# Optimization experiments

Hardware: AMD Instinct MI355X
Metric: run time of the kernel (lower is better)

Reference implementation:

```python
import jax, jax.numpy as jnp
import numpy as np

D_MODEL = 1024
N_HEAD = 16
D_HEAD = D_MODEL // N_HEAD
D_FF = 4096
EPS = 1e-5


def _layernorm(x, gamma, beta):
    mu = jnp.mean(x, axis=-1, keepdims=True)
    var = jnp.mean(jnp.square(x - mu), axis=-1, keepdims=True)
    return (x - mu) * jax.lax.rsqrt(var + EPS) * gamma + beta


def setup_inputs() -> dict:
    key = jax.random.key(0)
    ks = jax.random.split(key, 16)
    s = 1.0 / np.sqrt(D_MODEL)
    sf = 1.0 / np.sqrt(D_FF)
    return {
        "src": jax.random.normal(ks[0], (8, 1024, D_MODEL), dtype=jnp.float32),
        "Wq": jax.random.uniform(ks[1], (D_MODEL, D_MODEL), jnp.float32, -s, s),
        "bq": jnp.zeros((D_MODEL,), jnp.float32),
        "Wk": jax.random.uniform(ks[2], (D_MODEL, D_MODEL), jnp.float32, -s, s),
        "bk": jnp.zeros((D_MODEL,), jnp.float32),
        "Wv": jax.random.uniform(ks[3], (D_MODEL, D_MODEL), jnp.float32, -s, s),
        "bv": jnp.zeros((D_MODEL,), jnp.float32),
        "Wo": jax.random.uniform(ks[4], (D_MODEL, D_MODEL), jnp.float32, -s, s),
        "bo": jnp.zeros((D_MODEL,), jnp.float32),
        "W1": jax.random.uniform(ks[5], (D_MODEL, D_FF), jnp.float32, -s, s),
        "b1": jnp.zeros((D_FF,), jnp.float32),
        "W2": jax.random.uniform(ks[6], (D_FF, D_MODEL), jnp.float32, -sf, sf),
        "b2": jnp.zeros((D_MODEL,), jnp.float32),
        "g1": jnp.ones((D_MODEL,), jnp.float32),
        "beta1": jnp.zeros((D_MODEL,), jnp.float32),
        "g2": jnp.ones((D_MODEL,), jnp.float32),
        "beta2": jnp.zeros((D_MODEL,), jnp.float32),
    }


def reference(src, Wq, bq, Wk, bk, Wv, bv, Wo, bo, W1, b1, W2, b2, g1, beta1, g2, beta2):
    B, S, _ = src.shape
    x = _layernorm(src, g1, beta1)
    # QKV projections -> [B, H, S, Dh]
    def split_heads(t):
        return t.reshape(B, S, N_HEAD, D_HEAD).transpose(0, 2, 1, 3)
    q = split_heads(x @ Wq + bq)
    k = split_heads(x @ Wk + bk)
    v = split_heads(x @ Wv + bv)
    # SymbolicAttention (canonical graph): softmax(q k^T / sqrt(d_head)) v
    scores = jnp.einsum('bhqd,bhkd->bhqk', q, k) / np.sqrt(D_HEAD).astype(np.float32)
    attn = jax.nn.softmax(scores, axis=-1)
    ctx = jnp.einsum('bhqk,bhkd->bhqd', attn, v)
    ctx = ctx.transpose(0, 2, 1, 3).reshape(B, S, D_MODEL)
    src = src + (ctx @ Wo + bo)  # dropout is identity in eval
    y = _layernorm(src, g2, beta2)
    ffn = jax.nn.relu(y @ W1 + b1) @ W2 + b2
    return src + ffn
```

## Files before the change

### kernel.cpp

```cpp
#include <hip/hip_runtime.h>
#include <stdint.h>

#define D_MODEL 1024
#define N_HEAD  16
#define D_HEAD  64
#define D_FF    4096
#define SEQ     1024
#define BATCH   8
#define M_TOK   (BATCH*SEQ)

typedef __attribute__((ext_vector_type(8))) short bf16x8;
typedef __attribute__((ext_vector_type(4))) float f32x4;

__device__ __forceinline__ float bf2f(unsigned short u) {
    union { unsigned int u; float f; } x; x.u = ((unsigned int)u) << 16; return x.f;
}
__device__ __forceinline__ unsigned short f2bf(float f) {
    union { float f; unsigned int u; } x; x.f = f;
    unsigned int r = x.u + 0x7fffu + ((x.u >> 16) & 1u);
    return (unsigned short)(r >> 16);
}

typedef const __attribute__((address_space(1))) unsigned int* gas_t;
typedef __attribute__((address_space(3))) unsigned int* las_t;
__device__ __forceinline__ void gl_lds16(const unsigned short* g, unsigned short* l) {
    __builtin_amdgcn_global_load_lds((gas_t)g, (las_t)l, 16, 0, 0);
}

__global__ __launch_bounds__(256) void transpose_cvt(
        const float* __restrict__ src, unsigned short* __restrict__ dst,
        int R, int C)
{
    __shared__ float t[32][33];
    const int tx = threadIdx.x & 31, ty = threadIdx.x >> 5;
    const int c0 = blockIdx.x * 32, r0 = blockIdx.y * 32;
    #pragma unroll
    for (int i = 0; i < 32; i += 8)
        t[ty + i][tx] = src[(size_t)(r0 + ty + i) * C + c0 + tx];
    __syncthreads();
    #pragma unroll
    for (int i = 0; i < 32; i += 8)
        dst[(size_t)(c0 + ty + i) * R + r0 + tx] = f2bf(t[tx][ty + i]);
}

__global__ __launch_bounds__(256) void ln_kernel(
        const float* __restrict__ x, const float* __restrict__ g,
        const float* __restrict__ be, unsigned short* __restrict__ out)
{
    const int row = blockIdx.x, tid = threadIdx.x;
    const f32x4 v = *(const f32x4*)(x + (size_t)row * D_MODEL + tid * 4);
    float s  = v[0] + v[1] + v[2] + v[3];
    float ss = v[0]*v[0] + v[1]*v[1] + v[2]*v[2] + v[3]*v[3];
    #pragma unroll
    for (int o = 1; o < 64; o <<= 1) { s += __shfl_xor(s, o); ss += __shfl_xor(ss, o); }
    __shared__ float sa[4], sb[4];
    const int wv = tid >> 6;
    if ((tid & 63) == 0) { sa[wv] = s; sb[wv] = ss; }
    __syncthreads();
    s  = sa[0] + sa[1] + sa[2] + sa[3];
    ss = sb[0] + sb[1] + sb[2] + sb[3];
    const float mu   = s * (1.0f / D_MODEL);
    const float rstd = rsqrtf(ss * (1.0f / D_MODEL) - mu * mu + 1e-5f);
    const f32x4 gv = *(const f32x4*)(g  + tid * 4);
    const f32x4 bv = *(const f32x4*)(be + tid * 4);
    unsigned short w[4];
    #pragma unroll
    for (int j = 0; j < 4; j++) w[j] = f2bf((v[j] - mu) * rstd * gv[j] + bv[j]);
    *(uint2*)(out + (size_t)row * D_MODEL + tid * 4) = *(uint2*)w;
}

template<int MODE>
__global__ __launch_bounds__(512, 2) void gemm256(
        const unsigned short* __restrict__ A,
        const unsigned short* __restrict__ BT,
        const float* __restrict__ b1_,
        const float* __restrict__ b2_,
        const float* __restrict__ b3_,
        void* __restrict__ Cout,
        int M, int N, int K)
{
    (void)M;
    __shared__ unsigned short As[32768];
    __shared__ unsigned short Bs[32768];

    const int tid  = threadIdx.x;
    const int wave = tid >> 6, lane = tid & 63;
    const int quad = lane >> 4, l16 = lane & 15;
    const int wm = wave >> 2, wn = wave & 3;

    const int m0 = blockIdx.y * 256;
    const int n0 = blockIdx.x * 256;
    const int NT = K >> 6;

    const int st_row = tid >> 3;
    const int st_g   = (tid & 7) ^ (st_row & 7);
    const unsigned short* gA = A  + (size_t)(m0 + st_row) * K + st_g * 8;
    const unsigned short* gB = BT + (size_t)(n0 + st_row) * K + st_g * 8;
    unsigned short* lA = As + wave * 512;
    unsigned short* lB = Bs + wave * 512;

    const int aOff = (wm * 64 + l16) * 64;
    const int bOff = (wn * 32 + l16) * 64;
    const int s0s  = (quad ^ (l16 & 7)) * 8;
    const int s1s  = s0s ^ 32;

    f32x4 acc[8][4] = {};

#define STAGE_A(T, H, D) \
    do { gl_lds16(gA + (size_t)((H)*128   )*K + (size_t)(T)*64, lA + (D)*16384 + (H)*8192); \
         gl_lds16(gA + (size_t)((H)*128+64)*K + (size_t)(T)*64, lA + (D)*16384 + (H)*8192 + 4096); } while(0)
#define STAGE_B(T, H, D) \
    do { gl_lds16(gB + (size_t)((H)*128   )*K + (size_t)(T)*64, lB + (D)*16384 + (H)*8192); \
         gl_lds16(gB + (size_t)((H)*128+64)*K + (size_t)(T)*64, lB + (D)*16384 + (H)*8192 + 4096); } while(0)

    STAGE_A(0, 0, 0); STAGE_B(0, 0, 0); STAGE_B(0, 1, 0); STAGE_A(0, 1, 0);
    STAGE_A(1, 0, 1); STAGE_B(1, 0, 1); STAGE_B(1, 1, 1);
    asm volatile("s_waitcnt vmcnt(6)" ::: "memory");
    __builtin_amdgcn_s_barrier();
    asm volatile("" ::: "memory");

    for (int t = 0; t < NT; ++t) {
        const int db = t & 1;
        const unsigned short* Adb = As + db * 16384;
        const unsigned short* Bdb = Bs + db * 16384;
        bf16x8 af[4][2], bfA[2][2], bfB[2][2];

        #pragma unroll
        for (int mi = 0; mi < 4; ++mi) {
            af[mi][0] = *(const bf16x8*)(Adb + aOff + mi * 1024 + s0s);
            af[mi][1] = *(const bf16x8*)(Adb + aOff + mi * 1024 + s1s);
        }
        #pragma unroll
        for (int ni = 0; ni < 2; ++ni) {
            bfA[ni][0] = *(const bf16x8*)(Bdb + bOff + ni * 1024 + s0s);
            bfA[ni][1] = *(const bf16x8*)(Bdb + bOff + ni * 1024 + s1s);
        }
        if (t + 1 < NT) STAGE_A(t + 1, 1, db ^ 1);
        asm volatile("" ::: "memory");
        __builtin_amdgcn_s_barrier();
        asm volatile("s_waitcnt lgkmcnt(0)");
        __builtin_amdgcn_s_setprio(1);
        #pragma unroll
        for (int mi = 0; mi < 4; ++mi)
            #pragma unroll
            for (int ni = 0; ni < 2; ++ni) {
                acc[mi][ni] = __builtin_amdgcn_mfma_f32_16x16x32_bf16(
                        bfA[ni][0], af[mi][0], acc[mi][ni], 0, 0, 0);
                acc[mi][ni] = __builtin_amdgcn_mfma_f32_16x16x32_bf16(
                        bfA[ni][1], af[mi][1], acc[mi][ni], 0, 0, 0);
            }
        __builtin_amdgcn_s_setprio(0);
        asm volatile("" ::: "memory");
        __builtin_amdgcn_s_barrier();
        asm volatile("" ::: "memory");

        #pragma unroll
        for (int ni = 0; ni < 2; ++ni) {
            bfB[ni][0] = *(const bf16x8*)(Bdb + 8192 + bOff + ni * 1024 + s0s);
            bfB[ni][1] = *(const bf16x8*)(Bdb + 8192 + bOff + ni * 1024 + s1s);
        }
        if (t + 2 < NT) STAGE_A(t + 2, 0, db);
        asm volatile("" ::: "memory");
        __builtin_amdgcn_s_barrier();
        asm volatile("s_waitcnt lgkmcnt(0)");
        __builtin_amdgcn_s_setprio(1);
        #pragma unroll
        for (int mi = 0; mi < 4; ++mi)
            #pragma unroll
            for (int ni = 0; ni < 2; ++ni) {
                acc[mi][2 + ni] = __builtin_amdgcn_mfma_f32_16x16x32_bf16(
                        bfB[ni][0], af[mi][0], acc[mi][2 + ni], 0, 0, 0);
                acc[mi][2 + ni] = __builtin_amdgcn_mfma_f32_16x16x32_bf16(
                        bfB[ni][1], af[mi][1], acc[mi][2 + ni], 0, 0, 0);
            }
        __builtin_amdgcn_s_setprio(0);
        asm volatile("" ::: "memory");
        __builtin_amdgcn_s_barrier();
        asm volatile("" ::: "memory");

        #pragma unroll
        for (int mi = 0; mi < 4; ++mi) {
            af[mi][0] = *(const bf16x8*)(Adb + 8192 + aOff + mi * 1024 + s0s);
            af[mi][1] = *(const bf16x8*)(Adb + 8192 + aOff + mi * 1024 + s1s);
        }
        if (t + 2 < NT) STAGE_B(t + 2, 0, db);
        asm volatile("" ::: "memory");
        __builtin_amdgcn_s_barrier();
        asm volatile("s_waitcnt lgkmcnt(0)");
        __builtin_amdgcn_s_setprio(1);
        #pragma unroll
        for (int mi = 0; mi < 4; ++mi)
            #pragma unroll
            for (int ni = 0; ni < 2; ++ni) {
                acc[4 + mi][ni] = __builtin_amdgcn_mfma_f32_16x16x32_bf16(
                        bfA[ni][0], af[mi][0], acc[4 + mi][ni], 0, 0, 0);
                acc[4 + mi][ni] = __builtin_amdgcn_mfma_f32_16x16x32_bf16(
                        bfA[ni][1], af[mi][1], acc[4 + mi][ni], 0, 0, 0);
            }
        __builtin_amdgcn_s_setprio(0);
        asm volatile("" ::: "memory");
        __builtin_amdgcn_s_barrier();
        asm volatile("" ::: "memory");

        if (t + 2 < NT) {
            STAGE_B(t + 2, 1, db);
            asm volatile("s_waitcnt vmcnt(6)" ::: "memory");
        } else {
            asm volatile("s_waitcnt vmcnt(0)" ::: "memory");
        }
        __builtin_amdgcn_s_barrier();
        __builtin_amdgcn_s_setprio(1);
        #pragma unroll
        for (int mi = 0; mi < 4; ++mi)
            #pragma unroll
            for (int ni = 0; ni < 2; ++ni) {
                acc[4 + mi][2 + ni] = __builtin_amdgcn_mfma_f32_16x16x32_bf16(
                        bfB[ni][0], af[mi][0], acc[4 + mi][2 + ni], 0, 0, 0);
                acc[4 + mi][2 + ni] = __builtin_amdgcn_mfma_f32_16x16x32_bf16(
                        bfB[ni][1], af[mi][1], acc[4 + mi][2 + ni], 0, 0, 0);
            }
        __builtin_amdgcn_s_setprio(0);
        asm volatile("" ::: "memory");
        __builtin_amdgcn_s_barrier();
        asm volatile("" ::: "memory");
    }
#undef STAGE_A
#undef STAGE_B

    if (MODE == 1) {
        unsigned short* dst = (unsigned short*)Cout;
        #pragma unroll
        for (int f = 0; f < 8; ++f) {
            const int row = m0 + (f >> 2) * 128 + wm * 64 + (f & 3) * 16 + l16;
            #pragma unroll
            for (int g = 0; g < 4; ++g) {
                const int col = n0 + (g >> 1) * 128 + wn * 32 + (g & 1) * 16 + quad * 4;
                const f32x4 bs4 = *(const f32x4*)(b1_ + col);
                unsigned short w[4];
                #pragma unroll
                for (int r = 0; r < 4; ++r)
                    w[r] = f2bf(fmaxf(acc[f][g][r] + bs4[r], 0.0f));
                *(uint2*)(dst + (size_t)row * N + col) = *(uint2*)w;
            }
        }
    } else {
        const int rt = n0 >> 10;
        if (rt < 2) {
            unsigned short* dst = (unsigned short*)Cout + (size_t)rt * M_TOK * 1024;
            const float sc = (rt == 0) ? 0.125f : 1.0f;
            const float* bs = (rt == 0) ? b1_ : b2_;
            const int nb = n0 & 1023;
            #pragma unroll
            for (int f = 0; f < 8; ++f) {
                const int row = m0 + (f >> 2) * 128 + wm * 64 + (f & 3) * 16 + l16;
                #pragma unroll
                for (int g = 0; g < 4; ++g) {
                    const int col = nb + (g >> 1) * 128 + wn * 32 + (g & 1) * 16 + quad * 4;
                    const f32x4 bs4 = *(const f32x4*)(bs + col);
                    unsigned short w[4];
                    #pragma unroll
                    for (int r = 0; r < 4; ++r)
                        w[r] = f2bf((acc[f][g][r] + bs4[r]) * sc);
                    *(uint2*)(dst + (size_t)row * 1024 + col) = *(uint2*)w;
                }
            }
        } else {
            unsigned short* vdst = (unsigned short*)Cout + (size_t)2 * M_TOK * 1024;
            const int nb = n0 - 2048;
            #pragma unroll
            for (int f = 0; f < 8; ++f) {
                const int row = m0 + (f >> 2) * 128 + wm * 64 + (f & 3) * 16 + l16;
                const int bb = row >> 10, s = row & 1023;
                #pragma unroll
                for (int g = 0; g < 4; ++g) {
                    const int cc = nb + (g >> 1) * 128 + wn * 32 + (g & 1) * 16 + quad * 4;
                    #pragma unroll
                    for (int r = 0; r < 4; ++r)
                        vdst[((size_t)(bb * 1024 + cc + r)) * 1024 + s]
                            = f2bf(acc[f][g][r] + b3_[cc + r]);
                }
            }
        }
    }
}

template<int MODE>
__global__ __launch_bounds__(256) void gemm_bf16_tn(
        const unsigned short* __restrict__ A,
        const unsigned short* __restrict__ BT,
        const float* __restrict__ bias,
        const float* __restrict__ bias2,
        const float* __restrict__ bias3,
        const float* __restrict__ resid,
        void* __restrict__ Cout,
        int M, int N, int K)
{
    (void)bias2; (void)bias3;
    __shared__ unsigned short As[128 * 64];
    __shared__ unsigned short Bs[128 * 64];

    const int tid  = threadIdx.x;
    const int wave = tid >> 6, lane = tid & 63;
    const int quad = lane >> 4, l16 = lane & 15;

    int m0, n0;
    if (MODE == 2) {
        const int G = gridDim.x;
        const int f = blockIdx.x + G * blockIdx.y;
        m0 = ((f & 7) + 8 * ((f >> 3) / G)) * 128;
        n0 = ((f >> 3) % G) * 128;
    } else {
        m0 = blockIdx.y * 128;
        n0 = blockIdx.x * 128;
    }
    const int wm = (wave >> 1) * 64, wn = (wave & 1) * 64;

    const int st_row = wave * 8 + ((tid >> 3) & 7);
    const int st_g   = (tid & 7) ^ ((tid >> 3) & 7);
    const unsigned short* gA = A  + (size_t)(m0 + st_row) * K + st_g * 8;
    const unsigned short* gB = BT + (size_t)(n0 + st_row) * K + st_g * 8;
    unsigned short* lA = As + wave * 512;
    unsigned short* lB = Bs + wave * 512;
    const int rx = l16 & 7;

    f32x4 acc[4][4] = {};

    for (int k0 = 0; k0 < K; k0 += 64) {
        __syncthreads();
        #pragma unroll
        for (int j = 0; j < 4; j++) {
            gl_lds16(gA + (size_t)j * 32 * K + k0, lA + j * 2048);
            gl_lds16(gB + (size_t)j * 32 * K + k0, lB + j * 2048);
        }
        __syncthreads();

        #pragma unroll
        for (int h = 0; h < 2; h++) {
            bf16x8 af[4], bfr[4];
            #pragma unroll
            for (int mi = 0; mi < 4; mi++)
                af[mi] = *(const bf16x8*)(As + (wm + mi * 16 + l16) * 64
                                          + ((h * 4 + quad) ^ rx) * 8);
            #pragma unroll
            for (int ni = 0; ni < 4; ni++)
                bfr[ni] = *(const bf16x8*)(Bs + (wn + ni * 16 + l16) * 64
                                           + ((h * 4 + quad) ^ rx) * 8);
            #pragma unroll
            for (int mi = 0; mi < 4; mi++)
                #pragma unroll
                for (int ni = 0; ni < 4; ni++)
                    acc[mi][ni] = __builtin_amdgcn_mfma_f32_16x16x32_bf16(
                              bfr[ni], af[mi], acc[mi][ni], 0, 0, 0);
        }
    }

    #pragma unroll
    for (int mi = 0; mi < 4; mi++) {
        const int row = m0 + wm + mi * 16 + l16;
        #pragma unroll
        for (int ni = 0; ni < 4; ni++) {
            const int col = n0 + wn + ni * 16 + quad * 4;
            const f32x4 bs4 = *(const f32x4*)(bias + col);
            const f32x4 rv = *(const f32x4*)(resid + (size_t)row * N + col);
            f32x4 o;
            #pragma unroll
            for (int r = 0; r < 4; r++)
                o[r] = acc[mi][ni][r] + bs4[r] + rv[r];
            *(f32x4*)((float*)Cout + (size_t)row * N + col) = o;
        }
    }
}

#define ASTR 72
__global__ __launch_bounds__(256) void attn_mfma(
        const unsigned short* __restrict__ Q,
        const unsigned short* __restrict__ K,
        const unsigned short* __restrict__ VT,
        unsigned short* __restrict__ CTX)
{
    __shared__ unsigned short Ks[64 * ASTR];
    __shared__ unsigned short Vs[64 * ASTR];
    __shared__ unsigned short Ps[128 * ASTR];

    const int tid  = threadIdx.x;
    const int wave = tid >> 6, lane = tid & 63;
    const int quad = lane >> 4, l16 = lane & 15;
    const int bh = blockIdx.y;
    const int q0 = blockIdx.x * 128;
    const size_t baseQ = (size_t)(bh >> 4) * SEQ * D_MODEL + (size_t)(bh & 15) * D_HEAD;
    const size_t baseV = (size_t)bh * D_HEAD * SEQ;
    const int strip = wave * 32;

    bf16x8 qf[2][2];
    #pragma unroll
    for (int mt = 0; mt < 2; mt++)
        #pragma unroll
        for (int h = 0; h < 2; h++)
            qf[mt][h] = *(const bf16x8*)(Q + baseQ
                        + (size_t)(q0 + strip + mt * 16 + l16) * D_MODEL
                        + h * 32 + quad * 8);

    f32x4 of[2][4] = {};
    float l_p[2][4] = {};

    for (int c = 0; c < SEQ / 64; c++) {
        const int k0 = c * 64;
        __syncthreads();
        #pragma unroll
        for (int u = tid; u < 512; u += 256) {
            const int r = u >> 3, g = (u & 7) * 8;
            *(uint4*)(Ks + r * ASTR + g) =
                *(const uint4*)(K + baseQ + (size_t)(k0 + r) * D_MODEL + g);
            *(uint4*)(Vs + r * ASTR + g) =
                *(const uint4*)(VT + baseV + (size_t)r * SEQ + k0 + g);
        }
        __syncthreads();

        bf16x8 kf[4][2];
        #pragma unroll
        for (int kt = 0; kt < 4; kt++)
            #pragma unroll
            for (int h = 0; h < 2; h++)
                kf[kt][h] = *(const bf16x8*)(Ks + (kt * 16 + l16) * ASTR + h * 32 + quad * 8);

        #pragma unroll
        for (int mt = 0; mt < 2; mt++) {
            f32x4 s[4] = {};
            #pragma unroll
            for (int h = 0; h < 2; h++)
                #pragma unroll
                for (int kt = 0; kt < 4; kt++)
                    s[kt] = __builtin_amdgcn_mfma_f32_16x16x32_bf16(
                            qf[mt][h], kf[kt][h], s[kt], 0, 0, 0);
            #pragma unroll
            for (int kt = 0; kt < 4; kt++)
                #pragma unroll
                for (int r = 0; r < 4; r++) {
                    const float p = __expf(s[kt][r]);
                    l_p[mt][r] += p;
                    Ps[(strip + mt * 16 + quad * 4 + r) * ASTR + kt * 16 + l16] = f2bf(p);
                }
        }

        bf16x8 pf[2][2];
        #pragma unroll
        for (int mt = 0; mt < 2; mt++)
            #pragma unroll
            for (int h = 0; h < 2; h++)
                pf[mt][h] = *(const bf16x8*)(Ps + (strip + mt * 16 + l16) * ASTR
                                             + h * 32 + quad * 8);
        #pragma unroll
        for (int nt = 0; nt < 4; nt++) {
            bf16x8 vf[2];
            #pragma unroll
            for (int h = 0; h < 2; h++)
                vf[h] = *(const bf16x8*)(Vs + (nt * 16 + l16) * ASTR + h * 32 + quad * 8);
            #pragma unroll
            for (int mt = 0; mt < 2; mt++)
                #pragma unroll
                for (int h = 0; h < 2; h++)
                    of[mt][nt] = __builtin_amdgcn_mfma_f32_16x16x32_bf16(
                            pf[mt][h], vf[h], of[mt][nt], 0, 0, 0);
        }
    }

    #pragma unroll
    for (int mt = 0; mt < 2; mt++) {
        float inv[4];
        #pragma unroll
        for (int r = 0; r < 4; r++) {
            float l = l_p[mt][r];
            #pragma unroll
            for (int o = 1; o < 16; o <<= 1) l += __shfl_xor(l, o);
            inv[r] = 1.0f / l;
        }
        #pragma unroll
        for (int nt = 0; nt < 4; nt++)
            #pragma unroll
            for (int r = 0; r < 4; r++)
                CTX[baseQ + (size_t)(q0 + strip + mt * 16 + quad * 4 + r) * D_MODEL
                    + nt * 16 + l16] = f2bf(of[mt][nt][r] * inv[r]);
    }
}

extern "C" void kernel_launch(void* const* d_in, const int* in_sizes, int n_in,
                              void* d_out, int out_size, void* d_ws, size_t ws_size,
                              hipStream_t stream)
{
    (void)in_sizes; (void)n_in; (void)out_size; (void)ws_size;
    const float* src = (const float*)d_in[0];
    const float* Wq  = (const float*)d_in[1];
    const float* bq  = (const float*)d_in[2];
    const float* Wk  = (const float*)d_in[3];
    const float* bk  = (const float*)d_in[4];
    const float* Wv  = (const float*)d_in[5];
    const float* bv  = (const float*)d_in[6];
    const float* Wo  = (const float*)d_in[7];
    const float* bo  = (const float*)d_in[8];
    const float* W1  = (const float*)d_in[9];
    const float* b1  = (const float*)d_in[10];
    const float* W2  = (const float*)d_in[11];
    const float* b2  = (const float*)d_in[12];
    const float* g1  = (const float*)d_in[13];
    const float* be1 = (const float*)d_in[14];
    const float* g2  = (const float*)d_in[15];
    const float* be2 = (const float*)d_in[16];
    float* out = (float*)d_out;

    unsigned short* wqkvT = (unsigned short*)d_ws;
    unsigned short* woT = wqkvT + (size_t)3 * 1024 * 1024;
    unsigned short* w1T = woT + 1024 * 1024;
    unsigned short* w2T = w1T + (size_t)4096 * 1024;
    unsigned short* xn  = w2T + (size_t)1024 * 4096;
    unsigned short* q   = xn  + (size_t)M_TOK * D_MODEL;
    unsigned short* k   = q   + (size_t)M_TOK * D_MODEL;
    unsigned short* vT  = k   + (size_t)M_TOK * D_MODEL;
    unsigned short* ctx = vT  + (size_t)M_TOK * D_MODEL;
    unsigned short* hid = ctx + (size_t)M_TOK * D_MODEL;

    const dim3 blk(256);
    const dim3 blk512(512);

    transpose_cvt<<<dim3(32, 32),  blk, 0, stream>>>(Wq, wqkvT,                 1024, 1024);
    transpose_cvt<<<dim3(32, 32),  blk, 0, stream>>>(Wk, wqkvT + 1024 * 1024,   1024, 1024);
    transpose_cvt<<<dim3(32, 32),  blk, 0, stream>>>(Wv, wqkvT + 2 * 1024 * 1024, 1024, 1024);
    transpose_cvt<<<dim3(32, 32),  blk, 0, stream>>>(Wo, woT, 1024, 1024);
    transpose_cvt<<<dim3(128, 32), blk, 0, stream>>>(W1, w1T, 1024, 4096);
    transpose_cvt<<<dim3(32, 128), blk, 0, stream>>>(W2, w2T, 4096, 1024);

    ln_kernel<<<M_TOK, blk, 0, stream>>>(src, g1, be1, xn);

    gemm256<3><<<dim3(12, 32), blk512, 0, stream>>>(
        xn, wqkvT, bq, bk, bv, q, M_TOK, 3072, D_MODEL);

    attn_mfma<<<dim3(SEQ / 128, BATCH * N_HEAD), blk, 0, stream>>>(q, k, vT, ctx);

    gemm_bf16_tn<2><<<dim3(8, 64), blk, 0, stream>>>(
        ctx, woT, bo, nullptr, nullptr, src, out, M_TOK, D_MODEL, D_MODEL);

    ln_kernel<<<M_TOK, blk, 0, stream>>>(out, g2, be2, xn);

    gemm256<1><<<dim3(16, 32), blk512, 0, stream>>>(
        xn, w1T, b1, nullptr, nullptr, hid, M_TOK, D_FF, D_MODEL);

    gemm_bf16_tn<2><<<dim3(8, 64), blk, 0, stream>>>(
        hid, w2T, b2, nullptr, nullptr, out, out, M_TOK, D_MODEL, D_FF);
}
```

Measured before the change: 504.1 us.

## Use inline-asm LDS reads, reorder MFMAs, and remap blocks across XCDs in gemm256

The block index is remapped so consecutive tiles land in chunks per XCD (assuming 8 XCDs), which should improve L2 locality for shared A/B panels. LDS fragment loads become inline ds_read_b128 with immediate offsets from one base register, cutting address arithmetic. Sched barriers pin the order, and the MFMA loop order is changed so the two k-halves run as separate passes instead of back-to-back on the same accumulator. The asm reads hide dependencies from the compiler and assume the block count is divisible by 8.

```diff
diff --git a/kernel.cpp b/kernel.cpp
--- a/kernel.cpp
+++ b/kernel.cpp
@@ -26,6 +26,9 @@
 __device__ __forceinline__ void gl_lds16(const unsigned short* g, unsigned short* l) {
     __builtin_amdgcn_global_load_lds((gas_t)g, (las_t)l, 16, 0, 0);
 }
+
+#define DSR(dst, addr, IMM) \
+    asm volatile("ds_read_b128 %0, %1 offset:" #IMM : "=v"(dst) : "v"(addr))
 
 __global__ __launch_bounds__(256) void transpose_cvt(
         const float* __restrict__ src, unsigned short* __restrict__ dst,
@@ -88,8 +91,12 @@
     const int quad = lane >> 4, l16 = lane & 15;
     const int wm = wave >> 2, wn = wave & 3;
 
-    const int m0 = blockIdx.y * 256;
-    const int n0 = blockIdx.x * 256;
+    const int nbx = gridDim.x;
+    const int bid = blockIdx.x + nbx * blockIdx.y;
+    const int chunk = (nbx * gridDim.y) >> 3;
+    const int lg = (bid & 7) * chunk + (bid >> 3);
+    const int m0 = (lg / nbx) * 256;
+    const int n0 = (lg % nbx) * 256;
     const int NT = K >> 6;
 
     const int st_row = tid >> 3;
@@ -99,10 +106,12 @@
     unsigned short* lA = As + wave * 512;
     unsigned short* lB = Bs + wave * 512;
 
-    const int aOff = (wm * 64 + l16) * 64;
-    const int bOff = (wn * 32 + l16) * 64;
-    const int s0s  = (quad ^ (l16 & 7)) * 8;
-    const int s1s  = s0s ^ 32;
+    const unsigned asBase = (unsigned)(size_t)(las_t)(void*)As;
+    const unsigned bsBase = (unsigned)(size_t)(las_t)(void*)Bs;
+    const unsigned aOff = (unsigned)((wm * 64 + l16) * 128);
+    const unsigned bOff = (unsigned)((wn * 32 + l16) * 128);
+    const unsigned s0b  = (unsigned)((quad ^ (l16 & 7)) * 16);
+    const unsigned s1b  = s0b ^ 64;
 
     f32x4 acc[8][4] = {};
 
@@ -121,86 +130,90 @@
 
     for (int t = 0; t < NT; ++t) {
         const int db = t & 1;
-        const unsigned short* Adb = As + db * 16384;
-        const unsigned short* Bdb = Bs + db * 16384;
-        bf16x8 af[4][2], bfA[2][2], bfB[2][2];
-
-        #pragma unroll
-        for (int mi = 0; mi < 4; ++mi) {
-            af[mi][0] = *(const bf16x8*)(Adb + aOff + mi * 1024 + s0s);
-            af[mi][1] = *(const bf16x8*)(Adb + aOff + mi * 1024 + s1s);
-        }
-        #pragma unroll
-        for (int ni = 0; ni < 2; ++ni) {
-            bfA[ni][0] = *(const bf16x8*)(Bdb + bOff + ni * 1024 + s0s);
-            bfA[ni][1] = *(const bf16x8*)(Bdb + bOff + ni * 1024 + s1s);
-        }
+        const unsigned dbo = (unsigned)(db * 32768);
+        const unsigned aR0 = asBase + dbo + aOff + s0b;
+        const unsigned aR1 = asBase + dbo + aOff + s1b;
+        const unsigned bR0 = bsBase + dbo + bOff + s0b;
+        const unsigned bR1 = bsBase + dbo + bOff + s1b;
+        bf16x8 a0[4], a1[4], bA0[2], bA1[2], bB0[2], bB1[2];
+
+        DSR(a0[0], aR0, 0);    DSR(a0[1], aR0, 2048);
+        DSR(a0[2], aR0, 4096); DSR(a0[3], aR0, 6144);
+        DSR(a1[0], aR1, 0);    DSR(a1[1], aR1, 2048);
+        DSR(a1[2], aR1, 4096); DSR(a1[3], aR1, 6144);
+        DSR(bA0[0], bR0, 0);   DSR(bA0[1], bR0, 2048);
+        DSR(bA1[0], bR1, 0);   DSR(bA1[1], bR1, 2048);
         if (t + 1 < NT) STAGE_A(t + 1, 1, db ^ 1);
         asm volatile("" ::: "memory");
         __builtin_amdgcn_s_barrier();
-        asm volatile("s_waitcnt lgkmcnt(0)");
+        asm volatile("s_waitcnt lgkmcnt(0)" ::: "memory");
+        __builtin_amdgcn_sched_barrier(0);
         __builtin_amdgcn_s_setprio(1);
         #pragma unroll
         for (int mi = 0; mi < 4; ++mi)
             #pragma unroll
-            for (int ni = 0; ni < 2; ++ni) {
+            for (int ni = 0; ni < 2; ++ni)
                 acc[mi][ni] = __builtin_amdgcn_mfma_f32_16x16x32_bf16(
-                        bfA[ni][0], af[mi][0], acc[mi][ni], 0, 0, 0);
+                        bA0[ni], a0[mi], acc[mi][ni], 0, 0, 0);
+        #pragma unroll
+        for (int mi = 0; mi < 4; ++mi)
+            #pragma unroll
+            for (int ni = 0; ni < 2; ++ni)
                 acc[mi][ni] = __builtin_amdgcn_mfma_f32_16x16x32_bf16(
-                        bfA[ni][1], af[mi][1], acc[mi][ni], 0, 0, 0);
-            }
+                        bA1[ni], a1[mi], acc[mi][ni], 0, 0, 0);
         __builtin_amdgcn_s_setprio(0);
         asm volatile("" ::: "memory");
         __builtin_amdgcn_s_barrier();
-        asm volatile("" ::: "memory");
-
-        #pragma unroll
-        for (int ni = 0; ni < 2; ++ni) {
-            bfB[ni][0] = *(const bf16x8*)(Bdb + 8192 + bOff + ni * 1024 + s0s);
-            bfB[ni][1] = *(const bf16x8*)(Bdb + 8192 + bOff + ni * 1024 + s1s);
-        }
+
+        DSR(bB0[0], bR0, 16384);   DSR(bB0[1], bR0, 18432);
+        DSR(bB1[0], bR1, 16384);   DSR(bB1[1], bR1, 18432);
         if (t + 2 < NT) STAGE_A(t + 2, 0, db);
         asm volatile("" ::: "memory");
         __builtin_amdgcn_s_barrier();
-        asm volatile("s_waitcnt lgkmcnt(0)");
+        asm volatile("s_waitcnt lgkmcnt(0)" ::: "memory");
+        __builtin_amdgcn_sched_barrier(0);
         __builtin_amdgcn_s_setprio(1);
         #pragma unroll
         for (int mi = 0; mi < 4; ++mi)
             #pragma unroll
-            for (int ni = 0; ni < 2; ++ni) {
+            for (int ni = 0; ni < 2; ++ni)
                 acc[mi][2 + ni] = __builtin_amdgcn_mfma_f32_16x16x32_bf16(
-                        bfB[ni][0], af[mi][0], acc[mi][2 + ni], 0, 0, 0);
+                        bB0[ni], a0[mi], acc[mi][2 + ni], 0, 0, 0);
+        #pragma unroll
+        for (int mi = 0; mi < 4; ++mi)
+            #pragma unroll
+            for (int ni = 0; ni < 2; ++ni)
                 acc[mi][2 + ni] = __builtin_amdgcn_mfma_f32_16x16x32_bf16(
-                        bfB[ni][1], af[mi][1], acc[mi][2 + ni], 0, 0, 0);
-            }
+                        bB1[ni], a1[mi], acc[mi][2 + ni], 0, 0, 0);
         __builtin_amdgcn_s_setprio(0);
         asm volatile("" ::: "memory");
         __builtin_amdgcn_s_barrier();
-        asm volatile("" ::: "memory");
-
-        #pragma unroll
-        for (int mi = 0; mi < 4; ++mi) {
-            af[mi][0] = *(const bf16x8*)(Adb + 8192 + aOff + mi * 1024 + s0s);
-            af[mi][1] = *(const bf16x8*)(Adb + 8192 + aOff + mi * 1024 + s1s);
-        }
+
+        DSR(a0[0], aR0, 16384); DSR(a0[1], aR0, 18432);
+        DSR(a0[2], aR0, 20480); DSR(a0[3], aR0, 22528);
+        DSR(a1[0], aR1, 16384); DSR(a1[1], aR1, 18432);
+        DSR(a1[2], aR1, 20480); DSR(a1[3], aR1, 22528);
         if (t + 2 < NT) STAGE_B(t + 2, 0, db);
         asm volatile("" ::: "memory");
         __builtin_amdgcn_s_barrier();
-        asm volatile("s_waitcnt lgkmcnt(0)");
+        asm volatile("s_waitcnt lgkmcnt(0)" ::: "memory");
+        __builtin_amdgcn_sched_barrier(0);
         __builtin_amdgcn_s_setprio(1);
         #pragma unroll
         for (int mi = 0; mi < 4; ++mi)
             #pragma unroll
-            for (int ni = 0; ni < 2; ++ni) {
+            for (int ni = 0; ni < 2; ++ni)
                 acc[4 + mi][ni] = __builtin_amdgcn_mfma_f32_16x16x32_bf16(
-                        bfA[ni][0], af[mi][0], acc[4 + mi][ni], 0, 0, 0);
+                        bA0[ni], a0[mi], acc[4 + mi][ni], 0, 0, 0);
+        #pragma unroll
+        for (int mi = 0; mi < 4; ++mi)
+            #pragma unroll
+            for (int ni = 0; ni < 2; ++ni)
                 acc[4 + mi][ni] = __builtin_amdgcn_mfma_f32_16x16x32_bf16(
-                        bfA[ni][1], af[mi][1], acc[4 + mi][ni], 0, 0, 0);
-            }
+                        bA1[ni], a1[mi], acc[4 + mi][ni], 0, 0, 0);
         __builtin_amdgcn_s_setprio(0);
         asm volatile("" ::: "memory");
         __builtin_amdgcn_s_barrier();
-        asm volatile("" ::: "memory");
 
         if (t + 2 < NT) {
             STAGE_B(t + 2, 1, db);
@@ -213,16 +226,18 @@
         #pragma unroll
         for (int mi = 0; mi < 4; ++mi)
             #pragma unroll
-            for (int ni = 0; ni < 2; ++ni) {
+            for (int ni = 0; ni < 2; ++ni)
                 acc[4 + mi][2 + ni] = __builtin_amdgcn_mfma_f32_16x16x32_bf16(
-                        bfB[ni][0], af[mi][0], acc[4 + mi][2 + ni], 0, 0, 0);
+                        bB0[ni], a0[mi], acc[4 + mi][2 + ni], 0, 0, 0);
+        #pragma unroll
+        for (int mi = 0; mi < 4; ++mi)
+            #pragma unroll
+            for (int ni = 0; ni < 2; ++ni)
                 acc[4 + mi][2 + ni] = __builtin_amdgcn_mfma_f32_16x16x32_bf16(
-                        bfB[ni][1], af[mi][1], acc[4 + mi][2 + ni], 0, 0, 0);
-            }
+                        bB1[ni], a1[mi], acc[4 + mi][2 + ni], 0, 0, 0);
         __builtin_amdgcn_s_setprio(0);
         asm volatile("" ::: "memory");
         __builtin_amdgcn_s_barrier();
-        asm volatile("" ::: "memory");
     }
 #undef STAGE_A
 #undef STAGE_B
```

Result: no change. 497.4 us (-1.3%).
